# Kernel tuning notes

Hardware: AMD Instinct MI355X
Metric: run time of the kernel (lower is better)

The kernel has to match this reference:

```python
import jax, jax.numpy as jnp
import numpy as np
from jax import lax


def _dct_basis():
    # 64 separable 2D DCT-II basis filters, shape [64,1,8,8] (OIHW)
    k = 8
    a = np.full(k, np.sqrt(2.0 / k)); a[0] = np.sqrt(1.0 / k)
    u = np.arange(k)[:, None]; xx = np.arange(k)[None, :]
    B = a[:, None] * np.cos((2 * xx + 1) * u * np.pi / (2 * k))  # [u, x]
    basis = np.einsum('ux,vy->uvxy', B, B).reshape(64, 1, k, k)
    return jnp.asarray(basis, dtype=jnp.float32)


def _conv(x, w, b, pad):
    y = lax.conv_general_dilated(x, w, (1, 1), [(pad, pad), (pad, pad)],
                                 dimension_numbers=('NCHW', 'OIHW', 'NCHW'))
    return y + b[None, :, None, None]


def _bn(x, s, b, m, v, eps=1e-5):
    inv = s * lax.rsqrt(v + eps)
    return x * inv[None, :, None, None] + (b - m * inv)[None, :, None, None]


def _mp2(x):
    return lax.reduce_window(x, -jnp.inf, lax.max, (1, 1, 2, 2), (1, 1, 2, 2), 'VALID')


def setup_inputs() -> dict:
    key = jax.random.key(0)
    ks = jax.random.split(key, 32)
    B = 128
    d = {}
    d['x'] = jax.random.normal(ks[0], (B, 1, 256, 256), jnp.float32)
    d['qvectors'] = jax.random.uniform(ks[1], (B, 64), jnp.float32)
    d['dct_basis'] = _dct_basis()
    def w(k, shape, sc=0.02):
        return jax.random.normal(k, shape, jnp.float32) * sc
    # conv stack
    d['conv1a_w'] = w(ks[2], (64, 1, 5, 5));   d['conv1a_b'] = w(ks[3], (64,))
    d['conv1b_w'] = w(ks[4], (64, 64, 5, 5));  d['conv1b_b'] = w(ks[5], (64,))
    d['conv2a_w'] = w(ks[6], (128, 64, 5, 5)); d['conv2a_b'] = w(ks[7], (128,))
    d['conv3a_w'] = w(ks[8], (256, 128, 5, 5)); d['conv3a_b'] = w(ks[9], (256,))
    # batchnorm (eval-mode) params: scale, bias, running_mean, running_var
    for i, (name, c) in enumerate([('bn1a', 64), ('bn1b', 64), ('bn2a', 128), ('bn3a', 256)]):
        kk = jax.random.split(ks[10 + i], 4)
        d[name + '_s'] = 1.0 + w(kk[0], (c,))
        d[name + '_b'] = w(kk[1], (c,))
        d[name + '_m'] = w(kk[2], (c,))
        d[name + '_v'] = jax.random.uniform(kk[3], (c,), jnp.float32, 0.5, 1.5)
    d['fc1_w'] = w(ks[20], (500, 15 * 8 * 256 + 64), 0.01); d['fc1_b'] = w(ks[21], (500,))
    d['fc2_w'] = w(ks[22], (500, 564), 0.01);               d['fc2_b'] = w(ks[23], (500,))
    d['fc3_w'] = w(ks[24], (2, 564), 0.01);                 d['fc3_b'] = w(ks[25], (2,))
    return d


def reference(x, qvectors, dct_basis,
              conv1a_w, conv1a_b, bn1a_s, bn1a_b, bn1a_m, bn1a_v,
              conv1b_w, conv1b_b, bn1b_s, bn1b_b, bn1b_m, bn1b_v,
              conv2a_w, conv2a_b, bn2a_s, bn2a_b, bn2a_m, bn2a_v,
              conv3a_w, conv3a_b, bn3a_s, bn3a_b, bn3a_m, bn3a_v,
              fc1_w, fc1_b, fc2_w, fc2_b, fc3_w, fc3_b):
    gamma = 1e6
    # --- soft-histogram over DCT coefficients (no_grad in the original) ---
    dct = lax.conv_general_dilated(x, dct_basis, (8, 8), 'VALID',
                                   dimension_numbers=('NCHW', 'OIHW', 'NCHW'))  # [B,64,32,32]
    bins = jnp.arange(-60, 61, dtype=jnp.float32)  # 121 bins

    def step(_, b):
        s = jnp.sum(jax.nn.sigmoid(gamma * (dct - b)), axis=(2, 3)) / 1024.0  # [B,64]
        return None, s
    _, feats = lax.scan(step, None, bins)           # [121,B,64]
    feats = jnp.transpose(feats, (1, 0, 2))          # [B,121,64]
    features = feats[:, 0:120, :] - feats[:, 1:121, :]
    features = lax.stop_gradient(features.reshape(-1, 1, 120, 64))

    # --- CNN backbone ---
    h = jax.nn.relu(_bn(_conv(features, conv1a_w, conv1a_b, 2), bn1a_s, bn1a_b, bn1a_m, bn1a_v))
    h = jax.nn.relu(_bn(_conv(h, conv1b_w, conv1b_b, 2), bn1b_s, bn1b_b, bn1b_m, bn1b_v))
    h = _mp2(h)
    h = jax.nn.relu(_bn(_conv(h, conv2a_w, conv2a_b, 2), bn2a_s, bn2a_b, bn2a_m, bn2a_v))
    h = _mp2(h)
    h = jax.nn.relu(_bn(_conv(h, conv3a_w, conv3a_b, 2), bn3a_s, bn3a_b, bn3a_m, bn3a_v))
    h = _mp2(h)                                      # [B,256,15,8]
    h_flat = h.reshape(-1, 15 * 8 * 256)
    h = jnp.concatenate([qvectors, h_flat], axis=1)
    h = jax.nn.relu(h @ fc1_w.T + fc1_b)
    h = jnp.concatenate([qvectors, h], axis=1)
    h = jax.nn.relu(h @ fc2_w.T + fc2_b)
    h = jnp.concatenate([qvectors, h], axis=1)
    return h @ fc3_w.T + fc3_b
```

## Files before the change

kernel.cpp:

```cpp
#include <hip/hip_runtime.h>


typedef _Float16 half8 __attribute__((ext_vector_type(8)));
typedef _Float16 half4 __attribute__((ext_vector_type(4)));
typedef float f32x16 __attribute__((ext_vector_type(16)));

__device__ __forceinline__ void async_copy16(const void* g, void* l) {
  __builtin_amdgcn_global_load_lds(
      (__attribute__((address_space(1))) void*)g,
      (__attribute__((address_space(3))) void*)l, 16, 0, 0);
}

__global__ __launch_bounds__(256) void dct_kernel(const float* __restrict__ x,
                                                  const float* __restrict__ basis,
                                                  float* __restrict__ dct) {
  __shared__ __align__(16) float Bm[64];
  int tid = threadIdx.x;
  if (tid < 64) {
    int u = tid >> 3, xx = tid & 7;
    Bm[tid] = basis[(u * 8) * 64 + xx * 8] * 2.8284271247461903f;
  }
  __syncthreads();
  int gid = blockIdx.x * 256 + tid;
  int b = gid >> 10, blk = gid & 1023;
  int bi = blk >> 5, bj = blk & 31;
  const float* xp = x + (size_t)b * 65536 + (bi * 8) * 256 + bj * 8;
  float X[64];
#pragma unroll
  for (int r = 0; r < 8; ++r) {
    float4 p = *(const float4*)(xp + r * 256);
    float4 q = *(const float4*)(xp + r * 256 + 4);
    X[r * 8 + 0] = p.x; X[r * 8 + 1] = p.y; X[r * 8 + 2] = p.z; X[r * 8 + 3] = p.w;
    X[r * 8 + 4] = q.x; X[r * 8 + 5] = q.y; X[r * 8 + 6] = q.z; X[r * 8 + 7] = q.w;
  }
  float T[64];
#pragma unroll
  for (int u = 0; u < 8; ++u) {
    float t[8] = {0.f, 0.f, 0.f, 0.f, 0.f, 0.f, 0.f, 0.f};
#pragma unroll
    for (int xx = 0; xx < 8; ++xx) {
      float bm = Bm[u * 8 + xx];
#pragma unroll
      for (int y = 0; y < 8; ++y) t[y] += bm * X[xx * 8 + y];
    }
#pragma unroll
    for (int y = 0; y < 8; ++y) T[u * 8 + y] = t[y];
  }
  float* op = dct + (size_t)b * 65536 + bi * 32 + bj;
#pragma unroll
  for (int v = 0; v < 8; ++v) {
    float dc[8] = {0.f, 0.f, 0.f, 0.f, 0.f, 0.f, 0.f, 0.f};
#pragma unroll
    for (int y = 0; y < 8; ++y) {
      float bm = Bm[v * 8 + y];
#pragma unroll
      for (int u = 0; u < 8; ++u) dc[u] += bm * T[u * 8 + y];
    }
#pragma unroll
    for (int u = 0; u < 8; ++u) op[(u * 8 + v) * 1024] = dc[u];
  }
}

__global__ __launch_bounds__(256) void hist_kernel(const float* __restrict__ dct,
                                                   float* __restrict__ feat) {
  __shared__ __align__(16) float h[16 * 121];
  int tid = threadIdx.x;
  for (int i = tid; i < 16 * 121; i += 256) h[i] = 0.f;
  __syncthreads();
  int b = blockIdx.x >> 6, c = blockIdx.x & 63;
  const float* dp = dct + (size_t)(b * 64 + c) * 1024;
  float* hc = h + (tid & 15) * 121;
  float4 v4 = ((const float4*)dp)[tid];
  float vals[4] = {v4.x, v4.y, v4.z, v4.w};
#pragma unroll
  for (int i = 0; i < 4; ++i) {
    float d = vals[i];
    float fl = floorf(d);
    float t0 = d - fl;
    int k = (int)fl + 60;
    if (t0 >= 2e-5f && t0 <= 1.f - 1.2e-4f) {
      if (k >= 0 && k < 120) atomicAdd(hc + k, 1.0f);
    } else {
      float s0 = 1.f / (1.f + expf(-1e6f * t0));
      float s1 = 1.f / (1.f + expf(1e6f * (1.f - t0)));
      if (k >= 1 && k <= 120) atomicAdd(hc + k - 1, 1.f - s0);
      if (k >= 0 && k < 120)  atomicAdd(hc + k, s0 - s1);
      if (k >= -1 && k < 119) atomicAdd(hc + k + 1, s1);
    }
  }
  __syncthreads();
  for (int f = tid; f < 120; f += 256) {
    float s = 0.f;
#pragma unroll
    for (int l = 0; l < 16; ++l) s += h[l * 121 + f];
    feat[((size_t)b * 120 + f) * 64 + c] = s * (1.f / 1024.f);
  }
}

template <int CI, int CO>
__global__ __launch_bounds__(256) void wtrans(const float* __restrict__ w,
                                              _Float16* __restrict__ wt) {
  int i = blockIdx.x * 256 + threadIdx.x;
  if (i >= (CI / 8) * 30 * CO * 8) return;
  int c8 = i & 7;
  int t = i >> 3;
  int co = t % CO; t /= CO;
  int k = t % 30;
  int cg = t / 30;
  int ci = cg * 8 + c8;
  int kh = k / 6, kw = k % 6;
  float v = (kw < 5) ? w[((size_t)co * CI + ci) * 25 + kh * 5 + kw] : 0.f;
  wt[i] = (_Float16)v;
}

__global__ __launch_bounds__(256) void bnprep(const float* __restrict__ cb,
                                              const float* __restrict__ s,
                                              const float* __restrict__ b,
                                              const float* __restrict__ m,
                                              const float* __restrict__ v,
                                              float* __restrict__ scale,
                                              float* __restrict__ shift, int n) {
  int i = threadIdx.x;
  if (i < n) {
    float inv = s[i] * rsqrtf(v[i] + 1e-5f);
    scale[i] = inv;
    shift[i] = (cb[i] - m[i]) * inv + b[i];
  }
}

__global__ __launch_bounds__(256) void conv1a_f16(
    const float* __restrict__ in, const float* __restrict__ wts,
    const float* __restrict__ cb, const float* __restrict__ s_,
    const float* __restrict__ b_, const float* __restrict__ m_,
    const float* __restrict__ v_, _Float16* __restrict__ out) {
  __shared__ __align__(16) float wl[5 * 8 * 20];
  __shared__ __align__(16) float il[12 * 68];
  int tid = threadIdx.x, bid = blockIdx.x;
  int img = bid / 30;
  int r = bid % 30;
  int cob = r / 15;
  int h0 = (r % 15) * 8;
  int cog = tid & 7, wg = (tid >> 3) & 3, hh = tid >> 5;
  float acc[4][16];
#pragma unroll
  for (int i = 0; i < 4; ++i)
#pragma unroll
    for (int j = 0; j < 16; ++j) acc[i][j] = 0.f;
  for (int idx = tid; idx < 32 * 25; idx += 256) {
    int rr = idx % 25, co = idx / 25;
    float v = wts[(cob * 32 + co) * 25 + rr];
    int kh = rr / 5, kw = rr % 5;
    wl[(kh * 8 + (co >> 2)) * 20 + (co & 3) * 5 + kw] = v;
  }
  for (int idx = tid; idx < 12 * 68; idx += 256) {
    int cc = idx % 68, rr = idx / 68;
    int hy = h0 + rr - 2, wx = cc - 2;
    float v = 0.f;
    if (hy >= 0 && hy < 120 && wx >= 0 && wx < 64)
      v = in[(size_t)img * 7680 + hy * 64 + wx];
    il[idx] = v;
  }
  __syncthreads();
#pragma unroll
  for (int kh = 0; kh < 5; ++kh) {
    const float* ir = &il[(hh + kh) * 68 + wg * 16];
    float iv[20];
#pragma unroll
    for (int i = 0; i < 5; ++i) {
      float4 p = *(const float4*)(ir + i * 4);
      iv[i * 4] = p.x; iv[i * 4 + 1] = p.y; iv[i * 4 + 2] = p.z; iv[i * 4 + 3] = p.w;
    }
    const float* wr = &wl[(kh * 8 + cog) * 20];
    float wv[20];
#pragma unroll
    for (int i = 0; i < 5; ++i) {
      float4 p = *(const float4*)(wr + i * 4);
      wv[i * 4] = p.x; wv[i * 4 + 1] = p.y; wv[i * 4 + 2] = p.z; wv[i * 4 + 3] = p.w;
    }
#pragma unroll
    for (int co = 0; co < 4; ++co)
#pragma unroll
      for (int kw = 0; kw < 5; ++kw) {
        float w1 = wv[co * 5 + kw];
#pragma unroll
        for (int w = 0; w < 16; ++w) acc[co][w] += w1 * iv[w + kw];
      }
  }
  int h = h0 + hh;
  int co0 = cob * 32 + cog * 4;
  float inv[4], bia[4];
#pragma unroll
  for (int i = 0; i < 4; ++i) {
    int c = co0 + i;
    inv[i] = s_[c] * rsqrtf(v_[c] + 1e-5f);
    bia[i] = (cb[c] - m_[c]) * inv[i] + b_[c];
  }
  int g = co0 >> 3, off = co0 & 7;
  _Float16* op = out + (((size_t)(img * 8 + g) * 120 + h) * 64) * 8 + off;
#pragma unroll
  for (int w = 0; w < 16; ++w) {
    half4 o;
#pragma unroll
    for (int i = 0; i < 4; ++i)
      o[i] = (_Float16)fmaxf(acc[i][w] * inv[i] + bia[i], 0.f);
    *(half4*)&op[(size_t)(wg * 16 + w) * 8] = o;
  }
}

template <int CI, int CO, int H, int W, int BLK_M, bool OUT_NCHW>
__global__ __launch_bounds__(512) void conv5_mfma(
    const _Float16* __restrict__ in, const _Float16* __restrict__ wt,
    const float* __restrict__ scale, const float* __restrict__ shift,
    _Float16* __restrict__ out) {
  constexpr int NW_M = BLK_M / 64;
  constexpr int NW_N = 8 / NW_M;
  constexpr int BLK_N = NW_N * 128;
  constexpr int ROWS = BLK_N / W;
  constexpr int TB = (H + ROWS - 1) / ROWS;
  constexpr int NCOB = CO / BLK_M;
  constexpr int HR = ROWS + 4;
  constexpr int HC = W + 4;
  constexpr int CIG = CI / 8;
  constexpr int OH = H / 2, OW = W / 2;
  constexpr int AITER = (HR * HC + 511) / 512;
  constexpr int WBYTES = 30 * BLK_M * 16;
  constexpr int WITER = (WBYTES + 8191) / 8192;
  __shared__ __align__(16) _Float16 Alds[HR * HC * 8 + 8];
  __shared__ __align__(16) _Float16 Wlds[30 * BLK_M * 8];

  int tid = threadIdx.x;
  int bid = blockIdx.x;
  int img = bid / (TB * NCOB);
  int r = bid % (TB * NCOB);
  int tb = r / NCOB;
  int cob = r % NCOB;
  int h0 = tb * ROWS;

  int wid = tid >> 6, l = tid & 63, lo = l & 31, hi = l >> 5;
  int widM = wid / NW_N, widN = wid % NW_N;

  if (tid < 8) Alds[HR * HC * 8 + tid] = (_Float16)0.f;

  int wbase[2];
#pragma unroll
  for (int mi = 0; mi < 2; ++mi)
    wbase[mi] = (hi * BLK_M + widM * 64 + mi * 32 + lo) * 8;
  int bbase[4];
#pragma unroll
  for (int j = 0; j < 4; ++j) {
    int pix = widN * 128 + j * 32 + lo;
    bbase[j] = ((pix / W) * HC + (pix % W) + hi) * 8;
  }

  f32x16 acc[2][4];
#pragma unroll
  for (int mi = 0; mi < 2; ++mi)
#pragma unroll
    for (int j = 0; j < 4; ++j) acc[mi][j] = (f32x16){};

#pragma unroll 1
  for (int ci0 = 0; ci0 < CI; ci0 += 8) {
    int cg = ci0 >> 3;
    const _Float16* ing = in + (size_t)(img * CIG + cg) * H * W * 8;
    half8 areg[AITER];
#pragma unroll
    for (int it = 0; it < AITER; ++it) {
      int i = tid + it * 512;
      half8 v = {};
      if (i < HR * HC) {
        int rr = i / HC, cc = i % HC;
        int hy = h0 + rr - 2, wx = cc - 2;
        if (hy >= 0 && hy < H && wx >= 0 && wx < W)
          v = *(const half8*)&ing[(size_t)(hy * W + wx) * 8];
      }
      areg[it] = v;
    }
    const char* wsrc = (const char*)(wt + ((size_t)cg * 30 * CO + cob * BLK_M) * 8);
#pragma unroll
    for (int rr = 0; rr < WITER; ++rr) {
      int f = rr * 8192 + tid * 16;
      if (f < WBYTES) {
        int row = f / (BLK_M * 16);
        int off = f % (BLK_M * 16);
        async_copy16(wsrc + (size_t)row * (CO * 16) + off,
                     (char*)Wlds + (rr * 8192 + wid * 1024));
      }
    }
#pragma unroll
    for (int it = 0; it < AITER; ++it) {
      int i = tid + it * 512;
      if (i < HR * HC) *(half8*)&Alds[i * 8] = areg[it];
    }
    __syncthreads();
#pragma unroll
    for (int kh = 0; kh < 5; ++kh) {
#pragma unroll
      for (int kwb = 0; kwb < 3; ++kwb) {
        half8 af[2], bf[4];
#pragma unroll
        for (int mi = 0; mi < 2; ++mi)
          af[mi] = *(const half8*)&Wlds[wbase[mi] + (kh * 6 + 2 * kwb) * BLK_M * 8];
#pragma unroll
        for (int j = 0; j < 4; ++j)
          bf[j] = *(const half8*)&Alds[bbase[j] + (kh * HC + 2 * kwb) * 8];
#pragma unroll
        for (int mi = 0; mi < 2; ++mi)
#pragma unroll
          for (int j = 0; j < 4; ++j)
            acc[mi][j] = __builtin_amdgcn_mfma_f32_32x32x16_f16(
                af[mi], bf[j], acc[mi][j], 0, 0, 0);
      }
    }
    __syncthreads();
  }

  if (!OUT_NCHW) {
    constexpr int CGO = CO / 8;
    int gbase = (cob * BLK_M + widM * 64) >> 3;
    bool lane_ok = ((lo & 1) == 0);
#pragma unroll
    for (int mi = 0; mi < 2; ++mi) {
#pragma unroll
      for (int r4 = 0; r4 < 4; ++r4) {
        int g = gbase + mi * 4 + r4;
        int co0 = g * 8 + hi * 4;
        float4 sv = *(const float4*)&scale[co0];
        float4 tv = *(const float4*)&shift[co0];
        float sa[4] = {sv.x, sv.y, sv.z, sv.w};
        float ta[4] = {tv.x, tv.y, tv.z, tv.w};
#pragma unroll
        for (int p = 0; p < 2; ++p) {
          int ja = (W == 64) ? p : 2 * p;
          int jb = (W == 64) ? p + 2 : 2 * p + 1;
          int orow = (W == 64) ? (h0 >> 1) + widN : (h0 >> 1) + widN * 2 + p;
          int ocol = (W == 64) ? p * 16 + (lo >> 1) : (lo >> 1);
          half4 o;
#pragma unroll
          for (int c = 0; c < 4; ++c) {
            int reg = r4 * 4 + c;
            float v0 = fmaxf(acc[mi][ja][reg] * sa[c] + ta[c], 0.f);
            float v1 = fmaxf(acc[mi][jb][reg] * sa[c] + ta[c], 0.f);
            float m = fmaxf(v0, v1);
            m = fmaxf(m, __shfl_xor(m, 1, 64));
            o[c] = (_Float16)m;
          }
          if (lane_ok && orow < OH)
            *(half4*)&out[(((size_t)(img * CGO + g) * OH + orow) * OW + ocol) * 8 +
                          hi * 4] = o;
        }
      }
    }
  } else {
    bool lane_ok = ((lo & 1) == 0) && (lo < 16);
#pragma unroll
    for (int mi = 0; mi < 2; ++mi) {
#pragma unroll
      for (int reg = 0; reg < 16; ++reg) {
        int co = cob * BLK_M + widM * 64 + mi * 32 + (reg & 3) + 8 * (reg >> 2) + 4 * hi;
        float s = scale[co], t = shift[co];
#pragma unroll
        for (int j = 0; j < 4; ++j) {
          float v = fmaxf(acc[mi][j][reg] * s + t, 0.f);
          float m = fmaxf(v, __shfl_xor(v, 16, 64));
          m = fmaxf(m, __shfl_xor(m, 1, 64));
          int orow = (h0 >> 1) + widN * 4 + j;
          if (lane_ok && orow < OH)
            out[((size_t)(img * CO + co) * OH + orow) * OW + ((lo & 15) >> 1)] =
                (_Float16)m;
        }
      }
    }
  }
}

__global__ __launch_bounds__(256, 2) void fc1_mfma(const float* __restrict__ qv,
                                                   const _Float16* __restrict__ p3,
                                                   const float* __restrict__ w,
                                                   float* __restrict__ part) {
  __shared__ __align__(16) _Float16 Wl[8 * 256 * 8];
  __shared__ __align__(16) _Float16 Bl[8 * 128 * 8];
  int tid = threadIdx.x;
  int ks = blockIdx.x >> 1, mt = blockIdx.x & 1;
  int wid = tid >> 6, l = tid & 63, lo = l & 31, hi = l >> 5;
  f32x16 acc[2][4];
#pragma unroll
  for (int mi = 0; mi < 2; ++mi)
#pragma unroll
    for (int j = 0; j < 4; ++j) acc[mi][j] = (f32x16){};

#pragma unroll 1
  for (int i3 = 0; i3 < 3; ++i3) {
    int c = ks + 240 * i3;
    if (c > 480) break;
    for (int idx = tid; idx < 2048; idx += 256) {
      int n_loc = idx >> 3, k8 = idx & 7;
      int n = mt * 256 + n_loc;
      half8 v = {};
      if (n < 500) {
        const float* src = w + (size_t)n * 30784 + c * 64 + k8 * 8;
        float4 f0 = *(const float4*)src;
        float4 f1 = *(const float4*)(src + 4);
        v[0] = (_Float16)f0.x; v[1] = (_Float16)f0.y;
        v[2] = (_Float16)f0.z; v[3] = (_Float16)f0.w;
        v[4] = (_Float16)f1.x; v[5] = (_Float16)f1.y;
        v[6] = (_Float16)f1.z; v[7] = (_Float16)f1.w;
      }
      *(half8*)&Wl[(size_t)(k8 * 256 + n_loc) * 8] = v;
    }
    for (int idx = tid; idx < 1024; idx += 256) {
      int img = idx >> 3, k8 = idx & 7;
      half8 v;
      if (c == 0) {
        const float* src = qv + img * 64 + k8 * 8;
        float4 f0 = *(const float4*)src;
        float4 f1 = *(const float4*)(src + 4);
        v[0] = (_Float16)f0.x; v[1] = (_Float16)f0.y;
        v[2] = (_Float16)f0.z; v[3] = (_Float16)f0.w;
        v[4] = (_Float16)f1.x; v[5] = (_Float16)f1.y;
        v[6] = (_Float16)f1.z; v[7] = (_Float16)f1.w;
      } else {
        v = *(const half8*)&p3[(size_t)img * 30720 + (c * 64 - 64) + k8 * 8];
      }
      *(half8*)&Bl[(size_t)(k8 * 128 + img) * 8] = v;
    }
    __syncthreads();
#pragma unroll
    for (int ks16 = 0; ks16 < 4; ++ks16) {
      half8 af[2], bf[4];
#pragma unroll
      for (int mi = 0; mi < 2; ++mi)
        af[mi] = *(const half8*)&Wl[(size_t)((ks16 * 2 + hi) * 256 + wid * 64 +
                                             mi * 32 + lo) * 8];
#pragma unroll
      for (int j = 0; j < 4; ++j)
        bf[j] = *(const half8*)&Bl[(size_t)((ks16 * 2 + hi) * 128 + j * 32 + lo) * 8];
#pragma unroll
      for (int mi = 0; mi < 2; ++mi)
#pragma unroll
        for (int j = 0; j < 4; ++j)
          acc[mi][j] = __builtin_amdgcn_mfma_f32_32x32x16_f16(
              af[mi], bf[j], acc[mi][j], 0, 0, 0);
    }
    __syncthreads();
  }
#pragma unroll
  for (int mi = 0; mi < 2; ++mi)
#pragma unroll
    for (int reg = 0; reg < 16; ++reg) {
      int n = mt * 256 + wid * 64 + mi * 32 + (reg & 3) + 8 * (reg >> 2) + 4 * hi;
#pragma unroll
      for (int j = 0; j < 4; ++j)
        part[((size_t)ks * 512 + n) * 128 + j * 32 + lo] = acc[mi][j][reg];
    }
}

__global__ __launch_bounds__(256) void fc1_reduce(const float* __restrict__ part,
                                                  const float* __restrict__ bias,
                                                  float* __restrict__ out) {
  int idx = blockIdx.x * 256 + threadIdx.x;
  int img = idx & 127, n = idx >> 7;
  float s = 0.f;
#pragma unroll 8
  for (int ks = 0; ks < 240; ++ks) s += part[((size_t)ks * 512 + n) * 128 + img];
  out[n * 128 + img] = (n < 500) ? fmaxf(s + bias[n], 0.f) : 0.f;
}

__global__ __launch_bounds__(256) void fc2_kernel(const float* __restrict__ qv,
                                                  const float* __restrict__ fc1o,
                                                  const float* __restrict__ w,
                                                  const float* __restrict__ bias,
                                                  float* __restrict__ out) {
  int idx = blockIdx.x * 256 + threadIdx.x;
  if (idx >= 128 * 500) return;
  int m = idx & 127, n = idx >> 7;
  const float* wr = w + (size_t)n * 564;
  float acc = 0.f;
#pragma unroll 8
  for (int k = 0; k < 64; ++k) acc += qv[m * 64 + k] * wr[k];
#pragma unroll 4
  for (int k = 0; k < 500; ++k) acc += fc1o[k * 128 + m] * wr[64 + k];
  out[n * 128 + m] = fmaxf(acc + bias[n], 0.f);
}

__global__ __launch_bounds__(256) void fc3_kernel(const float* __restrict__ qv,
                                                  const float* __restrict__ fc2o,
                                                  const float* __restrict__ w,
                                                  const float* __restrict__ bias,
                                                  float* __restrict__ out) {
  int tid = threadIdx.x;
  int m = tid >> 1, n = tid & 1;
  const float* wr = w + (size_t)n * 564;
  float acc = 0.f;
#pragma unroll 8
  for (int k = 0; k < 64; ++k) acc += qv[m * 64 + k] * wr[k];
#pragma unroll 4
  for (int k = 0; k < 500; ++k) acc += fc2o[k * 128 + m] * wr[64 + k];
  out[m * 2 + n] = acc + bias[n];
}

extern "C" void kernel_launch(void* const* d_in, const int* in_sizes, int n_in,
                              void* d_out, int out_size, void* d_ws, size_t ws_size,
                              hipStream_t stream) {
  (void)in_sizes; (void)n_in; (void)out_size; (void)ws_size;
  const float* x      = (const float*)d_in[0];
  const float* qv     = (const float*)d_in[1];
  const float* basis  = (const float*)d_in[2];
  const float* c1aw   = (const float*)d_in[3];
  const float* c1ab   = (const float*)d_in[4];
  const float* c1bw   = (const float*)d_in[5];
  const float* c1bb   = (const float*)d_in[6];
  const float* c2aw   = (const float*)d_in[7];
  const float* c2ab   = (const float*)d_in[8];
  const float* c3aw   = (const float*)d_in[9];
  const float* c3ab   = (const float*)d_in[10];
  const float* bn1a_s = (const float*)d_in[11];
  const float* bn1a_b = (const float*)d_in[12];
  const float* bn1a_m = (const float*)d_in[13];
  const float* bn1a_v = (const float*)d_in[14];
  const float* bn1b_s = (const float*)d_in[15];
  const float* bn1b_b = (const float*)d_in[16];
  const float* bn1b_m = (const float*)d_in[17];
  const float* bn1b_v = (const float*)d_in[18];
  const float* bn2a_s = (const float*)d_in[19];
  const float* bn2a_b = (const float*)d_in[20];
  const float* bn2a_m = (const float*)d_in[21];
  const float* bn2a_v = (const float*)d_in[22];
  const float* bn3a_s = (const float*)d_in[23];
  const float* bn3a_b = (const float*)d_in[24];
  const float* bn3a_m = (const float*)d_in[25];
  const float* bn3a_v = (const float*)d_in[26];
  const float* fc1w   = (const float*)d_in[27];
  const float* fc1b   = (const float*)d_in[28];
  const float* fc2w   = (const float*)d_in[29];
  const float* fc2b   = (const float*)d_in[30];
  const float* fc3w   = (const float*)d_in[31];
  const float* fc3b   = (const float*)d_in[32];

  float* ws = (float*)d_ws;
  float* feat = ws;
  _Float16* wt1b = (_Float16*)(ws + 1000000);
  _Float16* wt2a = (_Float16*)(ws + 1070000);
  _Float16* wt3a = (_Float16*)(ws + 1200000);
  float* sc1b = ws + 1700000; float* sh1b = ws + 1700100;
  float* sc2a = ws + 1700200; float* sh2a = ws + 1700400;
  float* sc3a = ws + 1700600; float* sh3a = ws + 1701000;
  _Float16* p1 = (_Float16*)(ws + 1710000);
  float* S = ws + 9600000;
  float* dct     = S;
  _Float16* a1c  = (_Float16*)S;
  _Float16* p2   = (_Float16*)(ws + 25400000);
  _Float16* p3   = (_Float16*)(ws + 1710000);
  float* f1p  = S;
  float* f1o  = ws + 29400000;
  float* f2o  = ws + 29500000;

  wtrans<64, 64><<<480, 256, 0, stream>>>(c1bw, wt1b);
  wtrans<64, 128><<<960, 256, 0, stream>>>(c2aw, wt2a);
  wtrans<128, 256><<<3840, 256, 0, stream>>>(c3aw, wt3a);
  bnprep<<<1, 256, 0, stream>>>(c1bb, bn1b_s, bn1b_b, bn1b_m, bn1b_v, sc1b, sh1b, 64);
  bnprep<<<1, 256, 0, stream>>>(c2ab, bn2a_s, bn2a_b, bn2a_m, bn2a_v, sc2a, sh2a, 128);
  bnprep<<<1, 256, 0, stream>>>(c3ab, bn3a_s, bn3a_b, bn3a_m, bn3a_v, sc3a, sh3a, 256);

  dct_kernel<<<512, 256, 0, stream>>>(x, basis, dct);
  hist_kernel<<<128 * 64, 256, 0, stream>>>(dct, feat);

  for (int c = 0; c < 2; ++c) {
    const float* fin = feat + (size_t)c * 64 * 120 * 64;
    _Float16* pout = p1 + (size_t)c * 64 * 8 * 60 * 32 * 8;
    conv1a_f16<<<64 * 30, 256, 0, stream>>>(fin, c1aw, c1ab, bn1a_s, bn1a_b,
                                            bn1a_m, bn1a_v, a1c);
    conv5_mfma<64, 64, 120, 64, 64, false><<<64 * 8, 512, 0, stream>>>(
        a1c, wt1b, sc1b, sh1b, pout);
  }

  conv5_mfma<64, 128, 60, 32, 128, false><<<128 * 4, 512, 0, stream>>>(
      p1, wt2a, sc2a, sh2a, p2);

  conv5_mfma<128, 256, 30, 16, 128, true><<<128 * 2, 512, 0, stream>>>(
      p2, wt3a, sc3a, sh3a, p3);

  fc1_mfma<<<480, 256, 0, stream>>>(qv, p3, fc1w, f1p);
  fc1_reduce<<<256, 256, 0, stream>>>(f1p, fc1b, f1o);
  fc2_kernel<<<250, 256, 0, stream>>>(qv, f1o, fc2w, fc2b, f2o);
  fc3_kernel<<<1, 256, 0, stream>>>(qv, f2o, fc3w, fc3b, (float*)d_out);
}
```

Baseline: 814.0 us.

## Pack 5x5 taps into 13 MFMA steps and double-buffer conv3a LDS

The weight layout drops from 30 padded taps (6 per row) to 26 (25 taps plus one zero pad). Each MFMA k-step now covers two consecutive taps, with the per-half-wave activation offset taken from the tap index, so each input-channel group needs 13 MFMA steps instead of 15. For the conv3a instance, activations and weights are also double-buffered in LDS, so the next channel group's global loads and async weight copies overlap the current group's compute. The cost is twice the shared memory for that kernel, which may lower occupancy, plus some extra address computation per step.

```diff
diff --git a/kernel.cpp b/kernel.cpp
--- a/kernel.cpp
+++ b/kernel.cpp
@@ -101,15 +101,14 @@
 __global__ __launch_bounds__(256) void wtrans(const float* __restrict__ w,
                                               _Float16* __restrict__ wt) {
   int i = blockIdx.x * 256 + threadIdx.x;
-  if (i >= (CI / 8) * 30 * CO * 8) return;
+  if (i >= (CI / 8) * 26 * CO * 8) return;
   int c8 = i & 7;
   int t = i >> 3;
   int co = t % CO; t /= CO;
-  int k = t % 30;
-  int cg = t / 30;
+  int k = t % 26;
+  int cg = t / 26;
   int ci = cg * 8 + c8;
-  int kh = k / 6, kw = k % 6;
-  float v = (kw < 5) ? w[((size_t)co * CI + ci) * 25 + kh * 5 + kw] : 0.f;
+  float v = (k < 25) ? w[((size_t)co * CI + ci) * 25 + k] : 0.f;
   wt[i] = (_Float16)v;
 }
 
@@ -207,7 +206,7 @@
   }
 }
 
-template <int CI, int CO, int H, int W, int BLK_M, bool OUT_NCHW>
+template <int CI, int CO, int H, int W, int BLK_M, bool OUT_NCHW, bool DBUF>
 __global__ __launch_bounds__(512) void conv5_mfma(
     const _Float16* __restrict__ in, const _Float16* __restrict__ wt,
     const float* __restrict__ scale, const float* __restrict__ shift,
@@ -223,10 +222,13 @@
   constexpr int CIG = CI / 8;
   constexpr int OH = H / 2, OW = W / 2;
   constexpr int AITER = (HR * HC + 511) / 512;
-  constexpr int WBYTES = 30 * BLK_M * 16;
+  constexpr int WBYTES = 26 * BLK_M * 16;
   constexpr int WITER = (WBYTES + 8191) / 8192;
-  __shared__ __align__(16) _Float16 Alds[HR * HC * 8 + 8];
-  __shared__ __align__(16) _Float16 Wlds[30 * BLK_M * 8];
+  constexpr int NBUF = DBUF ? 2 : 1;
+  constexpr int ASZ = HR * HC * 8;
+  constexpr int WSZ = 26 * BLK_M * 8;
+  __shared__ __align__(16) _Float16 Alds[NBUF][ASZ];
+  __shared__ __align__(16) _Float16 Wlds[NBUF][WSZ];
 
   int tid = threadIdx.x;
   int bid = blockIdx.x;
@@ -239,8 +241,6 @@
   int wid = tid >> 6, l = tid & 63, lo = l & 31, hi = l >> 5;
   int widM = wid / NW_N, widN = wid % NW_N;
 
-  if (tid < 8) Alds[HR * HC * 8 + tid] = (_Float16)0.f;
-
   int wbase[2];
 #pragma unroll
   for (int mi = 0; mi < 2; ++mi)
@@ -249,7 +249,7 @@
 #pragma unroll
   for (int j = 0; j < 4; ++j) {
     int pix = widN * 128 + j * 32 + lo;
-    bbase[j] = ((pix / W) * HC + (pix % W) + hi) * 8;
+    bbase[j] = ((pix / W) * HC + (pix % W)) * 8;
   }
 
   f32x16 acc[2][4];
@@ -258,11 +258,8 @@
 #pragma unroll
     for (int j = 0; j < 4; ++j) acc[mi][j] = (f32x16){};
 
-#pragma unroll 1
-  for (int ci0 = 0; ci0 < CI; ci0 += 8) {
-    int cg = ci0 >> 3;
+  auto loadA = [&](int cg, half8* areg) {
     const _Float16* ing = in + (size_t)(img * CIG + cg) * H * W * 8;
-    half8 areg[AITER];
 #pragma unroll
     for (int it = 0; it < AITER; ++it) {
       int i = tid + it * 512;
@@ -275,7 +272,9 @@
       }
       areg[it] = v;
     }
-    const char* wsrc = (const char*)(wt + ((size_t)cg * 30 * CO + cob * BLK_M) * 8);
+  };
+  auto issueW = [&](int cg, int buf) {
+    const char* wsrc = (const char*)(wt + ((size_t)cg * 26 * CO + cob * BLK_M) * 8);
 #pragma unroll
     for (int rr = 0; rr < WITER; ++rr) {
       int f = rr * 8192 + tid * 16;
@@ -283,35 +282,68 @@
         int row = f / (BLK_M * 16);
         int off = f % (BLK_M * 16);
         async_copy16(wsrc + (size_t)row * (CO * 16) + off,
-                     (char*)Wlds + (rr * 8192 + wid * 1024));
-      }
-    }
+                     (char*)&Wlds[buf][0] + (rr * 8192 + wid * 1024));
+      }
+    }
+  };
+  auto writeA = [&](int buf, half8* areg) {
 #pragma unroll
     for (int it = 0; it < AITER; ++it) {
       int i = tid + it * 512;
-      if (i < HR * HC) *(half8*)&Alds[i * 8] = areg[it];
-    }
+      if (i < HR * HC) *(half8*)&Alds[buf][i * 8] = areg[it];
+    }
+  };
+  auto compute = [&](int buf) {
+#pragma unroll
+    for (int p = 0; p < 13; ++p) {
+      int pos1 = 2 * p + 1;
+      int off0 = ((2 * p) / 5) * HC + ((2 * p) % 5);
+      int off1 = (pos1 < 25) ? (pos1 / 5) * HC + (pos1 % 5) : 0;
+      int off = (hi ? off1 : off0) * 8;
+      half8 af[2], bf[4];
+#pragma unroll
+      for (int mi = 0; mi < 2; ++mi)
+        af[mi] = *(const half8*)&Wlds[buf][wbase[mi] + 2 * p * BLK_M * 8];
+#pragma unroll
+      for (int j = 0; j < 4; ++j)
+        bf[j] = *(const half8*)&Alds[buf][bbase[j] + off];
+#pragma unroll
+      for (int mi = 0; mi < 2; ++mi)
+#pragma unroll
+        for (int j = 0; j < 4; ++j)
+          acc[mi][j] = __builtin_amdgcn_mfma_f32_32x32x16_f16(
+              af[mi], bf[j], acc[mi][j], 0, 0, 0);
+    }
+  };
+
+  if constexpr (DBUF) {
+    half8 areg[AITER];
+    loadA(0, areg);
+    issueW(0, 0);
+    writeA(0, areg);
     __syncthreads();
-#pragma unroll
-    for (int kh = 0; kh < 5; ++kh) {
-#pragma unroll
-      for (int kwb = 0; kwb < 3; ++kwb) {
-        half8 af[2], bf[4];
-#pragma unroll
-        for (int mi = 0; mi < 2; ++mi)
-          af[mi] = *(const half8*)&Wlds[wbase[mi] + (kh * 6 + 2 * kwb) * BLK_M * 8];
-#pragma unroll
-        for (int j = 0; j < 4; ++j)
-          bf[j] = *(const half8*)&Alds[bbase[j] + (kh * HC + 2 * kwb) * 8];
-#pragma unroll
-        for (int mi = 0; mi < 2; ++mi)
-#pragma unroll
-          for (int j = 0; j < 4; ++j)
-            acc[mi][j] = __builtin_amdgcn_mfma_f32_32x32x16_f16(
-                af[mi], bf[j], acc[mi][j], 0, 0, 0);
-      }
-    }
-    __syncthreads();
+#pragma unroll 1
+    for (int cg = 0; cg < CIG; ++cg) {
+      int cur = cg & 1;
+      if (cg + 1 < CIG) {
+        loadA(cg + 1, areg);
+        issueW(cg + 1, cur ^ 1);
+      }
+      compute(cur);
+      if (cg + 1 < CIG) writeA(cur ^ 1, areg);
+      __syncthreads();
+    }
+  } else {
+#pragma unroll 1
+    for (int cg = 0; cg < CIG; ++cg) {
+      half8 areg[AITER];
+      loadA(cg, areg);
+      issueW(cg, 0);
+      writeA(0, areg);
+      __syncthreads();
+      compute(0);
+      __syncthreads();
+    }
   }
 
   if (!OUT_NCHW) {
@@ -554,9 +586,9 @@
   float* f1o  = ws + 29400000;
   float* f2o  = ws + 29500000;
 
-  wtrans<64, 64><<<480, 256, 0, stream>>>(c1bw, wt1b);
-  wtrans<64, 128><<<960, 256, 0, stream>>>(c2aw, wt2a);
-  wtrans<128, 256><<<3840, 256, 0, stream>>>(c3aw, wt3a);
+  wtrans<64, 64><<<416, 256, 0, stream>>>(c1bw, wt1b);
+  wtrans<64, 128><<<832, 256, 0, stream>>>(c2aw, wt2a);
+  wtrans<128, 256><<<3328, 256, 0, stream>>>(c3aw, wt3a);
   bnprep<<<1, 256, 0, stream>>>(c1bb, bn1b_s, bn1b_b, bn1b_m, bn1b_v, sc1b, sh1b, 64);
   bnprep<<<1, 256, 0, stream>>>(c2ab, bn2a_s, bn2a_b, bn2a_m, bn2a_v, sc2a, sh2a, 128);
   bnprep<<<1, 256, 0, stream>>>(c3ab, bn3a_s, bn3a_b, bn3a_m, bn3a_v, sc3a, sh3a, 256);
@@ -569,14 +601,14 @@
     _Float16* pout = p1 + (size_t)c * 64 * 8 * 60 * 32 * 8;
     conv1a_f16<<<64 * 30, 256, 0, stream>>>(fin, c1aw, c1ab, bn1a_s, bn1a_b,
                                             bn1a_m, bn1a_v, a1c);
-    conv5_mfma<64, 64, 120, 64, 64, false><<<64 * 8, 512, 0, stream>>>(
+    conv5_mfma<64, 64, 120, 64, 64, false, false><<<64 * 8, 512, 0, stream>>>(
         a1c, wt1b, sc1b, sh1b, pout);
   }
 
-  conv5_mfma<64, 128, 60, 32, 128, false><<<128 * 4, 512, 0, stream>>>(
+  conv5_mfma<64, 128, 60, 32, 128, false, false><<<128 * 4, 512, 0, stream>>>(
       p1, wt2a, sc2a, sh2a, p2);
 
-  conv5_mfma<128, 256, 30, 16, 128, true><<<128 * 2, 512, 0, stream>>>(
+  conv5_mfma<128, 256, 30, 16, 128, true, true><<<128 * 2, 512, 0, stream>>>(
       p2, wt3a, sc3a, sh3a, p3);
 
   fc1_mfma<<<480, 256, 0, stream>>>(qv, p3, fc1w, f1p);
```

After: 781.3 us. 4.0% less time.
